# Optimization experiments

Hardware: AMD Instinct MI355X
Metric: run time of the kernel (lower is better)

The kernel has to match this reference:

```python
import jax, jax.numpy as jnp
import numpy as np

ENC, PRED, JOINT_H, VOCAB, BLANK, MAXSYM = 1024, 320, 512, 29, 28, 6


def _lstm_step(x, h, c, Wi, Wh, b):
    # torch LSTM gate order: i, f, g, o
    gates = x @ Wi.T + h @ Wh.T + b
    i, f, g, o = jnp.split(gates, 4, axis=-1)
    c2 = jax.nn.sigmoid(f) * c + jax.nn.sigmoid(i) * jnp.tanh(g)
    h2 = jax.nn.sigmoid(o) * jnp.tanh(c2)
    return h2, c2


def setup_inputs() -> dict:
    key = jax.random.key(0)
    ks = jax.random.split(key, 13)
    B, T = 32, 48
    s = 0.1
    return {
        "x": jax.random.normal(ks[0], (B, T, ENC), jnp.float32),
        "out_lens": jax.random.randint(ks[1], (B,), T // 2, T + 1),
        "emb": s * jax.random.normal(ks[2], (VOCAB - 1, PRED), jnp.float32),
        "Wi0": s * jax.random.normal(ks[3], (4 * PRED, PRED), jnp.float32),
        "Wh0": s * jax.random.normal(ks[4], (4 * PRED, PRED), jnp.float32),
        "b0": s * jax.random.normal(ks[5], (4 * PRED,), jnp.float32),
        "Wi1": s * jax.random.normal(ks[6], (4 * PRED, PRED), jnp.float32),
        "Wh1": s * jax.random.normal(ks[7], (4 * PRED, PRED), jnp.float32),
        "b1": s * jax.random.normal(ks[8], (4 * PRED,), jnp.float32),
        "Wj1": s * jax.random.normal(ks[9], (JOINT_H, ENC + PRED), jnp.float32),
        "bj1": s * jax.random.normal(ks[10], (JOINT_H,), jnp.float32),
        "Wj2": s * jax.random.normal(ks[11], (VOCAB, JOINT_H), jnp.float32),
        "bj2": s * jax.random.normal(ks[12], (VOCAB,), jnp.float32),
    }


def reference(x, out_lens, emb, Wi0, Wh0, b0, Wi1, Wh1, b1, Wj1, bj1, Wj2, bj2):
    B, T, _ = x.shape
    rows = jnp.arange(B)
    n_steps = T * MAXSYM  # upper bound on greedy-loop iterations

    def pred_step(label, h, c):
        # SOS (-1) -> zero embedding, matching model.prediction(None, ...)
        e = jnp.where((label >= 0)[:, None], emb[jnp.clip(label, 0)], 0.0)
        h0, c0 = _lstm_step(e, h[0], c[0], Wi0, Wh0, b0)
        h1, c1 = _lstm_step(h0, h[1], c[1], Wi1, Wh1, b1)
        return h1, jnp.stack([h0, h1]), jnp.stack([c0, c1])

    def joint(f, g):
        z = jnp.concatenate([f, g], axis=-1)  # [B, ENC+PRED]
        return jax.nn.relu(z @ Wj1.T + bj1) @ Wj2.T + bj2  # [B, VOCAB]

    def body(state, _):
        h, c, lt, lc, f, ti, sa = state
        last = lt[rows, lc]                      # last emitted symbol (or -1 = SOS)
        g, h_p, c_p = pred_step(last, h, c)
        logits = joint(f, g)
        k = jnp.argmax(logits, axis=-1).astype(jnp.int32)
        blankness = k == BLANK
        ti = ti + blankness.astype(jnp.int32)
        blank_vec = ti >= out_lens               # finished sequences
        sa = sa * (~blankness)                   # reset symbol count on blank
        not_blank = ~(blank_vec | blankness)
        # masked hidden-state scatter: hidden[:, idx, :] = hidden_prime[:, idx, :]
        h = jnp.where(not_blank[None, :, None], h_p, h)
        c = jnp.where(not_blank[None, :, None], c_p, c)
        lc = lc + not_blank.astype(jnp.int32)
        # index_put_ accumulate of (k - SOS) into label tensor initialized to SOS=-1
        lt = lt.at[rows, lc].add(jnp.where(not_blank, k + 1, 0))
        sa = sa + not_blank.astype(jnp.int32)
        need_add = sa >= MAXSYM                  # force time advance at max symbols
        ti = ti + need_add.astype(jnp.int32)
        sa = sa * (sa < MAXSYM)
        # data-dependent re-fetch of encoder frame (clamped like time_idxs.min(max_lens))
        f = x[rows, jnp.minimum(ti, T - 1)]
        return (h, c, lt, lc, f, ti, sa), None

    h0 = jnp.zeros((2, B, PRED), x.dtype)
    c0 = jnp.zeros((2, B, PRED), x.dtype)
    lt0 = jnp.full((B, n_steps), -1, jnp.int32)
    lc0 = jnp.zeros((B,), jnp.int32)
    ti0 = jnp.zeros((B,), jnp.int32)
    sa0 = jnp.zeros((B,), jnp.int32)
    f0 = x[:, 0, :]
    state, _ = jax.lax.scan(body, (h0, c0, lt0, lc0, f0, ti0, sa0), None, length=n_steps)
    _, _, lt, lc, _, _, _ = state
    # labels for item i are lt[i, 1:lc[i]+1]; return padded tensor + lengths
    return lt, lc
```

## Files before the change

### kernel.cpp

```cpp
#include <hip/hip_runtime.h>
#include <math.h>

#define B_ 32
#define T_ 48
#define ENC_ 1024
#define PRED_ 320
#define JH_ 512
#define NJ_ 1344
#define VOCAB_ 29
#define BLANK_ 28
#define MAXSYM_ 6
#define NSTEPS_ 288
#define BDEC 512
#define GRID_DEC 160
#define NG 8
#define GBAT 4
#define NBLK 20
#define JPB 16
#define NJB 16
#define VPB 32
#define HPAD 324

#define FPRE_OFF 0
#define WE_OFF   786432
#define H0C2_OFF 822272
#define H1C2_OFF 842752
#define PL2_OFF  863232
#define INT_OFF  928768
#define NTAGS    2560
#define STAMPF   106496

__device__ __forceinline__ float sigm(float v) { return 1.0f / (1.0f + expf(-v)); }

__device__ __forceinline__ int  ld_i(const int* p)   { return __hip_atomic_load((int*)p, __ATOMIC_RELAXED, __HIP_MEMORY_SCOPE_AGENT); }
__device__ __forceinline__ void st_i(int* p, int v)  { __hip_atomic_store(p, v, __ATOMIC_RELAXED, __HIP_MEMORY_SCOPE_AGENT); }

__device__ __forceinline__ void st_pair(float* p, float v, int stamp) {
    float2 x; x.x = v; x.y = __int_as_float(stamp);
    asm volatile("global_store_dwordx2 %0, %1, off sc0 sc1" :: "v"(p), "v"(x) : "memory");
}
__device__ __forceinline__ void ldc4_2(const float* p0, const float* p1,
                                       float4& r0, float4& r1) {
    asm volatile("global_load_dwordx4 %0, %2, off sc0 sc1\n\t"
                 "global_load_dwordx4 %1, %3, off sc0 sc1\n\t"
                 "s_waitcnt vmcnt(0)"
                 : "=&v"(r0), "=&v"(r1)
                 : "v"(p0), "v"(p1)
                 : "memory");
}
__device__ __forceinline__ void ld2x4(const float* p0, const float* p1,
                                      const float* p2, const float* p3,
                                      float2& r0, float2& r1, float2& r2, float2& r3) {
    asm volatile("global_load_dwordx2 %0, %4, off sc0 sc1\n\t"
                 "global_load_dwordx2 %1, %5, off sc0 sc1\n\t"
                 "global_load_dwordx2 %2, %6, off sc0 sc1\n\t"
                 "global_load_dwordx2 %3, %7, off sc0 sc1\n\t"
                 "s_waitcnt vmcnt(0)"
                 : "=&v"(r0), "=&v"(r1), "=&v"(r2), "=&v"(r3)
                 : "v"(p0), "v"(p1), "v"(p2), "v"(p3)
                 : "memory");
}

#define PIDX(g, ks, jl, gb) ((((g)*8 + (ks))*16 + (jl))*4 + (gb))

__global__ void k_init(float* __restrict__ ws, int* __restrict__ out) {
    int idx = blockIdx.x * blockDim.x + threadIdx.x;
    int stride = gridDim.x * blockDim.x;
    for (int i = idx; i < STAMPF; i += stride) ws[H0C2_OFF + i] = 0.0f;
    int* wi = (int*)ws;
    for (int i = idx; i < NTAGS; i += stride) wi[INT_OFF + i] = 0;
    for (int i = idx; i < B_*NSTEPS_; i += stride) out[i] = -1;
    if (idx < B_) out[B_*NSTEPS_ + idx] = 0;
}

__global__ __launch_bounds__(256) void k_we(const float* __restrict__ emb,
                                            const float* __restrict__ Wi0,
                                            float* __restrict__ ws) {
    __shared__ float es[PRED_];
    int l = blockIdx.x / 5;
    int rq = blockIdx.x % 5;
    int t = threadIdx.x;
    if (t < PRED_) es[t] = emb[l*PRED_ + t];
    if (t + 256 < PRED_) es[t + 256] = emb[l*PRED_ + t + 256];
    __syncthreads();
    int r = rq*256 + t;
    const float4* wr = (const float4*)(Wi0 + (size_t)r*PRED_);
    float acc = 0.0f;
    #pragma unroll 4
    for (int k4 = 0; k4 < PRED_/4; ++k4) {
        float4 w = wr[k4];
        acc += w.x*es[4*k4] + w.y*es[4*k4+1] + w.z*es[4*k4+2] + w.w*es[4*k4+3];
    }
    ws[WE_OFF + l*(4*PRED_) + r] = acc;
}

__global__ __launch_bounds__(256) void k_fpre(const float* __restrict__ x,
                                              const float* __restrict__ Wj1,
                                              const float* __restrict__ bj1,
                                              float* __restrict__ ws) {
    __shared__ float As[B_][129];
    __shared__ float Bs[64][129];
    int tt = blockIdx.x >> 3;
    int jb = blockIdx.x & 7;
    int tid = threadIdx.x;
    int b = tid >> 3, jq = tid & 7;
    float acc[8] = {0,0,0,0,0,0,0,0};
    for (int kc = 0; kc < ENC_; kc += 128) {
        for (int i = tid; i < B_*128; i += 256) {
            int bb = i >> 7, kk = i & 127;
            As[bb][kk] = x[((size_t)bb*T_ + tt)*ENC_ + kc + kk];
        }
        for (int i = tid; i < 64*128; i += 256) {
            int jj = i >> 7, kk = i & 127;
            Bs[jj][kk] = Wj1[((size_t)(jb*64 + jj))*NJ_ + kc + kk];
        }
        __syncthreads();
        for (int kk = 0; kk < 128; ++kk) {
            float a = As[b][kk];
            #pragma unroll
            for (int u = 0; u < 8; ++u) acc[u] += a * Bs[jq*8 + u][kk];
        }
        __syncthreads();
    }
    #pragma unroll
    for (int u = 0; u < 8; ++u) {
        int j = jb*64 + jq*8 + u;
        ws[FPRE_OFF + ((size_t)b*T_ + tt)*JH_ + j] = acc[u] + bj1[j];
    }
}

__global__ __launch_bounds__(BDEC) void k_decode(
    const int* __restrict__ out_lens,
    const float* __restrict__ Wh0, const float* __restrict__ b0,
    const float* __restrict__ Wi1, const float* __restrict__ Wh1,
    const float* __restrict__ b1,
    const float* __restrict__ Wj1,
    const float* __restrict__ Wj2, const float* __restrict__ bj2,
    float* __restrict__ ws, int* __restrict__ out)
{
    const int tid = threadIdx.x;
    const int grp = blockIdx.x & 7;
    const int lb  = blockIdx.x >> 3;
    const int j0  = lb * JPB;
    const int v0  = lb * VPB;
    const int bb0 = grp * GBAT;

    float* H0C2g = ws + H0C2_OFF + grp*2560;
    float* H1C2g = ws + H1C2_OFF + grp*2560;
    float* PL2g  = ws + PL2_OFF  + grp*8192;
    const float* WE = ws + WE_OFF;
    const float* FP = ws + FPRE_OFF;
    int* wi = (int*)ws;
    int* tagD = wi + INT_OFF + grp*320;

    __shared__ __align__(16) float wi1_s[64*HPAD];
    __shared__ __align__(16) float hs0[GBAT*HPAD];
    __shared__ __align__(16) float hs1[GBAT*HPAD];
    __shared__ float parts[2048];
    __shared__ float parts2[2048];
    __shared__ float P0a[256], P0b[256], P1s[256];
    __shared__ float c0cur[64], c0cand[64], c1cur[64], c1cand[64];
    __shared__ float we_s[28][64];
    __shared__ float b0_s[64], b1_s[64], bj2_s[32];
    __shared__ float wj2t[VPB*33];
    __shared__ float jg_c[VPB*GBAT];
    __shared__ float hid_s[GBAT*33];
    __shared__ float logits_s[GBAT*33];
    __shared__ int ti_l[GBAT], last_l[GBAT], sa_l[GBAT], lc_l[GBAT], olen_s[GBAT];
    __shared__ unsigned s_masks[2];

    for (int i = tid; i < 64*PRED_; i += BDEC) {
        int r = i / PRED_, c = i % PRED_;
        int g = r >> 4, jj = r & 15;
        wi1_s[r*HPAD + c] = Wi1[((size_t)(g*PRED_ + j0 + jj))*PRED_ + c];
    }
    if (lb < NJB) {
        for (int i = tid; i < VPB*32; i += BDEC) {
            int v = i >> 5, l = i & 31;
            wj2t[v*33 + l] = (l < VOCAB_) ? Wj2[(size_t)l*JH_ + v0 + v] : 0.f;
        }
    }
    for (int i = tid; i < 28*64; i += BDEC) {
        int ls = i >> 6, r = i & 63;
        int g = r >> 4, jj = r & 15;
        we_s[ls][r] = WE[(size_t)ls*(4*PRED_) + g*PRED_ + j0 + jj];
    }
    if (tid < 64) {
        int g = tid >> 4, jj = tid & 15;
        b0_s[tid] = b0[g*PRED_ + j0 + jj];
        b1_s[tid] = b1[g*PRED_ + j0 + jj];
        c0cur[tid]=0.f; c0cand[tid]=0.f; c1cur[tid]=0.f; c1cand[tid]=0.f;
    }
    if (tid < VOCAB_) bj2_s[tid] = bj2[tid];
    if (tid < GBAT) {
        olen_s[tid] = out_lens[bb0 + tid];
        ti_l[tid] = 0; last_l[tid] = -1; sa_l[tid] = 0; lc_l[tid] = 0;
    }
    for (int i = tid; i < GBAT*HPAD; i += BDEC) { hs0[i] = 0.f; hs1[i] = 0.f; }
    if (tid < 256) P0a[tid] = 0.f;
    __syncthreads();

    const int gb  = tid & 3;
    const int jl  = (tid >> 2) & 15;
    const int ks  = tid >> 6;
    unsigned nbm = 0xfu, actm = 0xfu;

    for (int s = 0; s < NSTEPS_; ++s) {
        const int par = s & 1;
        const int st = s + 1;

        float f_reg = 0.f;
        if (lb < NJB && tid < 128) {
            int v_ = tid & 31, g2_ = tid >> 5;
            if ((actm >> g2_) & 1) {
                int tm = min(ti_l[g2_], T_ - 1);
                f_reg = FP[((size_t)(bb0+g2_)*T_ + tm)*JH_ + v0 + v_];
            }
        }

        if (nbm) {
            if (tid < 64) {
                int g2 = tid & 3, jj = tid >> 2;
                if ((nbm >> g2) & 1) {
                    int ls = last_l[g2];
                    float gt[4];
                    #pragma unroll
                    for (int g = 0; g < 4; ++g) {
                        int r = g*16 + jj;
                        float v = P0a[r*4 + g2] + b0_s[r];
                        if (ls >= 0) v += we_s[ls][r];
                        gt[g] = v;
                    }
                    float cn = sigm(gt[1])*c0cur[tid] + sigm(gt[0])*tanhf(gt[2]);
                    float hn = sigm(gt[3])*tanhf(cn);
                    c0cand[tid] = cn;
                    hs0[g2*HPAD + j0 + jj] = hn;
                    st_pair(&H0C2g[(lb*64 + tid)*2], hn, st);
                }
            }
            {
                const float* hr = &hs1[gb*HPAD];
                int k0 = ks * 40;
                float a0=0.f,a1=0.f,a2=0.f,a3=0.f;
                const float* w0 = Wh1 + ((size_t)(0*PRED_ + j0 + jl))*PRED_;
                const float* w1 = Wh1 + ((size_t)(1*PRED_ + j0 + jl))*PRED_;
                const float* w2 = Wh1 + ((size_t)(2*PRED_ + j0 + jl))*PRED_;
                const float* w3 = Wh1 + ((size_t)(3*PRED_ + j0 + jl))*PRED_;
                #pragma unroll 10
                for (int kk = k0; kk < k0 + 40; kk += 4) {
                    float4 h = *(const float4*)&hr[kk];
                    float4 q0 = *(const float4*)(w0 + kk);
                    float4 q1 = *(const float4*)(w1 + kk);
                    float4 q2 = *(const float4*)(w2 + kk);
                    float4 q3 = *(const float4*)(w3 + kk);
                    a0 += q0.x*h.x+q0.y*h.y+q0.z*h.z+q0.w*h.w;
                    a1 += q1.x*h.x+q1.y*h.y+q1.z*h.z+q1.w*h.w;
                    a2 += q2.x*h.x+q2.y*h.y+q2.z*h.z+q2.w*h.w;
                    a3 += q3.x*h.x+q3.y*h.y+q3.z*h.z+q3.w*h.w;
                }
                parts[PIDX(0,ks,jl,gb)] = a0;
                parts[PIDX(1,ks,jl,gb)] = a1;
                parts[PIDX(2,ks,jl,gb)] = a2;
                parts[PIDX(3,ks,jl,gb)] = a3;
            }
            __syncthreads();
            if (tid < 256) {
                int r = tid >> 2, g2 = tid & 3;
                int g = r >> 4, jj = r & 15;
                float v = 0.f;
                #pragma unroll
                for (int k = 0; k < 8; ++k) v += parts[PIDX(g,k,jj,g2)];
                P1s[r*4 + g2] = v;
            }
            {
                int b = tid >> 4, jj = tid & 15;
                if (tid < 320 && b != lb) {
                    const bool n0=(nbm>>0)&1, n1=(nbm>>1)&1, n2=(nbm>>2)&1, n3=(nbm>>3)&1;
                    const float* a0 = H0C2g + tid*8;
                    const float* a1 = a0 + 4;
                    float4 r0, r1;
                    for (;;) {
                        ldc4_2(a0, a1, r0, r1);
                        bool ok = (!n0 || __float_as_int(r0.y)==st)
                               && (!n1 || __float_as_int(r0.w)==st)
                               && (!n2 || __float_as_int(r1.y)==st)
                               && (!n3 || __float_as_int(r1.w)==st);
                        if (ok) break;
                        __builtin_amdgcn_s_sleep(1);
                    }
                    if (n0) hs0[0*HPAD + b*16 + jj] = r0.x;
                    if (n1) hs0[1*HPAD + b*16 + jj] = r0.z;
                    if (n2) hs0[2*HPAD + b*16 + jj] = r1.x;
                    if (n3) hs0[3*HPAD + b*16 + jj] = r1.z;
                }
            }
            __syncthreads();

            {
                const float* hr = &hs0[gb*HPAD];
                int k0 = ks * 40;
                float a0=0.f,a1=0.f,a2=0.f,a3=0.f;
                #pragma unroll 10
                for (int kk = k0; kk < k0 + 40; kk += 4) {
                    float4 h = *(const float4*)&hr[kk];
                    float4 q0 = *(const float4*)&wi1_s[(0*16+jl)*HPAD + kk];
                    float4 q1 = *(const float4*)&wi1_s[(1*16+jl)*HPAD + kk];
                    float4 q2 = *(const float4*)&wi1_s[(2*16+jl)*HPAD + kk];
                    float4 q3 = *(const float4*)&wi1_s[(3*16+jl)*HPAD + kk];
                    a0 += q0.x*h.x+q0.y*h.y+q0.z*h.z+q0.w*h.w;
                    a1 += q1.x*h.x+q1.y*h.y+q1.z*h.z+q1.w*h.w;
                    a2 += q2.x*h.x+q2.y*h.y+q2.z*h.z+q2.w*h.w;
                    a3 += q3.x*h.x+q3.y*h.y+q3.z*h.z+q3.w*h.w;
                }
                parts[PIDX(0,ks,jl,gb)] = a0;
                parts[PIDX(1,ks,jl,gb)] = a1;
                parts[PIDX(2,ks,jl,gb)] = a2;
                parts[PIDX(3,ks,jl,gb)] = a3;
            }
            __syncthreads();
            if (tid < 64) {
                int g2 = tid & 3, jj = tid >> 2;
                if ((nbm >> g2) & 1) {
                    float gt[4];
                    #pragma unroll
                    for (int g = 0; g < 4; ++g) {
                        int r = g*16 + jj;
                        float v = P1s[r*4 + g2] + b1_s[r];
                        #pragma unroll
                        for (int k = 0; k < 8; ++k) v += parts[PIDX(g,k,jj,g2)];
                        gt[g] = v;
                    }
                    float cn = sigm(gt[1])*c1cur[tid] + sigm(gt[0])*tanhf(gt[2]);
                    float hn = sigm(gt[3])*tanhf(cn);
                    c1cand[tid] = cn;
                    hs1[g2*HPAD + j0 + jj] = hn;
                    st_pair(&H1C2g[(lb*64 + tid)*2], hn, st);
                }
            }
            {
                const float* hr = &hs0[gb*HPAD];
                int k0 = ks * 40;
                float a0=0.f,a1=0.f,a2=0.f,a3=0.f;
                const float* w0 = Wh0 + ((size_t)(0*PRED_ + j0 + jl))*PRED_;
                const float* w1 = Wh0 + ((size_t)(1*PRED_ + j0 + jl))*PRED_;
                const float* w2 = Wh0 + ((size_t)(2*PRED_ + j0 + jl))*PRED_;
                const float* w3 = Wh0 + ((size_t)(3*PRED_ + j0 + jl))*PRED_;
                #pragma unroll 10
                for (int kk = k0; kk < k0 + 40; kk += 4) {
                    float4 h = *(const float4*)&hr[kk];
                    float4 q0 = *(const float4*)(w0 + kk);
                    float4 q1 = *(const float4*)(w1 + kk);
                    float4 q2 = *(const float4*)(w2 + kk);
                    float4 q3 = *(const float4*)(w3 + kk);
                    a0 += q0.x*h.x+q0.y*h.y+q0.z*h.z+q0.w*h.w;
                    a1 += q1.x*h.x+q1.y*h.y+q1.z*h.z+q1.w*h.w;
                    a2 += q2.x*h.x+q2.y*h.y+q2.z*h.z+q2.w*h.w;
                    a3 += q3.x*h.x+q3.y*h.y+q3.z*h.z+q3.w*h.w;
                }
                parts2[PIDX(0,ks,jl,gb)] = a0;
                parts2[PIDX(1,ks,jl,gb)] = a1;
                parts2[PIDX(2,ks,jl,gb)] = a2;
                parts2[PIDX(3,ks,jl,gb)] = a3;
            }
            {
                int b = tid >> 4, jj = tid & 15;
                if (tid < 320 && b != lb) {
                    const bool n0=(nbm>>0)&1, n1=(nbm>>1)&1, n2=(nbm>>2)&1, n3=(nbm>>3)&1;
                    const float* a0 = H1C2g + tid*8;
                    const float* a1 = a0 + 4;
                    float4 r0, r1;
                    for (;;) {
                        ldc4_2(a0, a1, r0, r1);
                        bool ok = (!n0 || __float_as_int(r0.y)==st)
                               && (!n1 || __float_as_int(r0.w)==st)
                               && (!n2 || __float_as_int(r1.y)==st)
                               && (!n3 || __float_as_int(r1.w)==st);
                        if (ok) break;
                        __builtin_amdgcn_s_sleep(1);
                    }
                    if (n0) hs1[0*HPAD + b*16 + jj] = r0.x;
                    if (n1) hs1[1*HPAD + b*16 + jj] = r0.z;
                    if (n2) hs1[2*HPAD + b*16 + jj] = r1.x;
                    if (n3) hs1[3*HPAD + b*16 + jj] = r1.z;
                }
            }
            __syncthreads();
        } else {
            if (lb < NJB) {
                if (tid < NBLK) { while (ld_i(&tagD[tid*16]) < s-1) __builtin_amdgcn_s_sleep(1); }
                __syncthreads();
            }
        }

        if (lb < NJB) {
            if (nbm) {
                int v = tid & 31, g2 = (tid >> 5) & 3, ks2 = tid >> 7;
                if ((nbm >> g2) & 1) {
                    const float* hr = &hs1[g2*HPAD];
                    const float* wt = Wj1 + ((size_t)(v0 + v))*NJ_ + ENC_ + ks2*80;
                    const float* hk = hr + ks2*80;
                    float p = 0.f;
                    #pragma unroll 20
                    for (int kk = 0; kk < 80; kk += 4) {
                        float4 w4 = *(const float4*)(wt + kk);
                        float4 h  = *(const float4*)(hk + kk);
                        p += w4.x*h.x + w4.y*h.y + w4.z*h.z + w4.w*h.w;
                    }
                    parts[(v*4 + g2)*4 + ks2] = p;
                }
            }
            __syncthreads();
            if (tid < 128) {
                int v = tid & 31, g2 = tid >> 5;
                if (nbm && ((nbm >> g2) & 1)) {
                    jg_c[v*4 + g2] = parts[(v*4+g2)*4+0] + parts[(v*4+g2)*4+1]
                                   + parts[(v*4+g2)*4+2] + parts[(v*4+g2)*4+3];
                }
                if ((actm >> g2) & 1) {
                    hid_s[g2*33 + v] = fmaxf(f_reg + jg_c[v*4 + g2], 0.f);
                }
            }
            __syncthreads();
            if (tid < 128) {
                int g2 = tid >> 5, l = tid & 31;
                const float* hb = &hid_s[g2*33];
                float acc = 0.f;
                #pragma unroll 8
                for (int v = 0; v < VPB; ++v) acc += wj2t[v*33 + l] * hb[v];
                st_pair(&PL2g[par*4096 + (lb*128 + tid)*2], acc, st);
            }
        }

        if (nbm && tid < 256) {
            int r = tid >> 2, g2 = tid & 3;
            int g = r >> 4, jj = r & 15;
            float v = 0.f;
            #pragma unroll
            for (int k = 0; k < 8; ++k) v += parts2[PIDX(g,k,jj,g2)];
            P0b[r*4 + g2] = v;
        }

        {
            int lb4 = tid >> 7, slot = tid & 127;
            const float* base = PL2g + par*4096 + (lb4*4*128 + slot)*2;
            float2 q0, q1, q2, q3;
            for (;;) {
                ld2x4(base, base + 256, base + 512, base + 768, q0, q1, q2, q3);
                if (__float_as_int(q0.y)==st && __float_as_int(q1.y)==st &&
                    __float_as_int(q2.y)==st && __float_as_int(q3.y)==st) break;
                __builtin_amdgcn_s_sleep(1);
            }
            parts[tid] = ((q0.x + q1.x) + q2.x) + q3.x;
        }
        __syncthreads();
        if (tid < 128) {
            float v = ((parts[tid] + parts[128+tid]) + parts[256+tid]) + parts[384+tid];
            int g2 = tid >> 5, l = tid & 31;
            logits_s[g2*33 + l] = (l < VOCAB_) ? (v + bj2_s[l]) : -1e30f;
        }
        __syncthreads();

        if (tid < 64) {
            bool nbb = false, actb = false;
            if (tid < GBAT && ((actm >> tid) & 1)) {
                const int g2 = tid;
                float best = -1e30f; int bi = 0;
                for (int l = 0; l < VOCAB_; ++l) {
                    float v = logits_s[g2*33 + l];
                    if (v > best) { best = v; bi = l; }
                }
                const int blankness = (bi == BLANK_) ? 1 : 0;
                int tiv = ti_l[g2] + blankness;
                if (tiv >= olen_s[g2]) {
                    ti_l[g2] = tiv;
                } else {
                    int notb = 1 - blankness;
                    int sav = blankness ? 0 : sa_l[g2];
                    int nl = last_l[g2];
                    int lcn = lc_l[g2];
                    if (notb) {
                        lcn += 1;
                        if (lb == g2) {
                            int bglob = bb0 + g2;
                            if (lcn < NSTEPS_) st_i(&out[bglob*NSTEPS_ + lcn], bi);
                            st_i(&out[B_*NSTEPS_ + bglob], lcn);
                        }
                        nl = bi;
                        sav += 1;
                    }
                    if (sav >= MAXSYM_) { tiv += 1; sav = 0; }
                    ti_l[g2] = tiv; sa_l[g2] = sav; last_l[g2] = nl; lc_l[g2] = lcn;
                    nbb = (notb != 0); actb = true;
                }
            }
            unsigned long long bn = __ballot(nbb);
            unsigned long long ba = __ballot(actb);
            if (tid == 0) { s_masks[0] = (unsigned)bn; s_masks[1] = (unsigned)ba; }
        }
        __syncthreads();
        const unsigned nbm_new = s_masks[0];
        actm = s_masks[1];
        if (tid < 64) {
            if ((nbm_new >> (tid & 3)) & 1) { c0cur[tid] = c0cand[tid]; c1cur[tid] = c1cand[tid]; }
        }
        if (tid < 256) {
            if ((nbm_new >> (tid & 3)) & 1) P0a[tid] = P0b[tid];
        }
        __syncthreads();
        nbm = nbm_new;
        if (tid == 0) st_i(&tagD[lb*16], s + 1);
        if (!actm) break;
    }
}

extern "C" void kernel_launch(void* const* d_in, const int* in_sizes, int n_in,
                              void* d_out, int out_size, void* d_ws, size_t ws_size,
                              hipStream_t stream) {
    const float* x    = (const float*)d_in[0];
    const int*   olen = (const int*)d_in[1];
    const float* emb  = (const float*)d_in[2];
    const float* Wi0  = (const float*)d_in[3];
    const float* Wh0  = (const float*)d_in[4];
    const float* b0   = (const float*)d_in[5];
    const float* Wi1  = (const float*)d_in[6];
    const float* Wh1  = (const float*)d_in[7];
    const float* b1   = (const float*)d_in[8];
    const float* Wj1  = (const float*)d_in[9];
    const float* bj1  = (const float*)d_in[10];
    const float* Wj2  = (const float*)d_in[11];
    const float* bj2  = (const float*)d_in[12];
    float* ws = (float*)d_ws;
    int* out = (int*)d_out;

    hipLaunchKernelGGL(k_init, dim3(256), dim3(256), 0, stream, ws, out);
    hipLaunchKernelGGL(k_we,   dim3(28*5), dim3(256), 0, stream, emb, Wi0, ws);
    hipLaunchKernelGGL(k_fpre, dim3(T_*8), dim3(256), 0, stream, x, Wj1, bj1, ws);
    hipLaunchKernelGGL(k_decode, dim3(GRID_DEC), dim3(BDEC), 0, stream,
                       olen, Wh0, b0, Wi1, Wh1, b1, Wj1, Wj2, bj2, ws, out);
}
```

Baseline: 4.422 ms.

## Restructure cross-block polling and overlap Wh1 matvec with logits gather

Cross-block spin-wait loads for the layer-0 and layer-1 hidden states are consolidated onto 128 threads, each polling five contiguous dwordx4 slots. The reductions of partial sums run concurrently on the other threads. The Wh1 recurrent matvec for the next step moves after the joint stage so it overlaps the logits exchange. The logits gather now reads contiguous vectors and reduces over 16 partials, with parts zeroed at init. The intent is fewer barriers and less serialized polling latency per greedy step. The cost is reordered data dependencies and an extra barrier before the layer-1 gather.

New measurement: 5.819 ms. 1.32x slower.

```diff
diff --git a/kernel.cpp b/kernel.cpp
--- a/kernel.cpp
+++ b/kernel.cpp
@@ -39,25 +39,29 @@
     float2 x; x.x = v; x.y = __int_as_float(stamp);
     asm volatile("global_store_dwordx2 %0, %1, off sc0 sc1" :: "v"(p), "v"(x) : "memory");
 }
-__device__ __forceinline__ void ldc4_2(const float* p0, const float* p1,
-                                       float4& r0, float4& r1) {
-    asm volatile("global_load_dwordx4 %0, %2, off sc0 sc1\n\t"
-                 "global_load_dwordx4 %1, %3, off sc0 sc1\n\t"
-                 "s_waitcnt vmcnt(0)"
-                 : "=&v"(r0), "=&v"(r1)
-                 : "v"(p0), "v"(p1)
-                 : "memory");
-}
-__device__ __forceinline__ void ld2x4(const float* p0, const float* p1,
-                                      const float* p2, const float* p3,
-                                      float2& r0, float2& r1, float2& r2, float2& r3) {
-    asm volatile("global_load_dwordx2 %0, %4, off sc0 sc1\n\t"
-                 "global_load_dwordx2 %1, %5, off sc0 sc1\n\t"
-                 "global_load_dwordx2 %2, %6, off sc0 sc1\n\t"
-                 "global_load_dwordx2 %3, %7, off sc0 sc1\n\t"
+__device__ __forceinline__ void ldc4_4(const float* p0, const float* p1,
+                                       const float* p2, const float* p3,
+                                       float4& r0, float4& r1, float4& r2, float4& r3) {
+    asm volatile("global_load_dwordx4 %0, %4, off sc0 sc1\n\t"
+                 "global_load_dwordx4 %1, %5, off sc0 sc1\n\t"
+                 "global_load_dwordx4 %2, %6, off sc0 sc1\n\t"
+                 "global_load_dwordx4 %3, %7, off sc0 sc1\n\t"
                  "s_waitcnt vmcnt(0)"
                  : "=&v"(r0), "=&v"(r1), "=&v"(r2), "=&v"(r3)
                  : "v"(p0), "v"(p1), "v"(p2), "v"(p3)
+                 : "memory");
+}
+__device__ __forceinline__ void ldc4_5(const float* p0, const float* p1, const float* p2,
+                                       const float* p3, const float* p4,
+                                       float4& r0, float4& r1, float4& r2, float4& r3, float4& r4) {
+    asm volatile("global_load_dwordx4 %0, %5, off sc0 sc1\n\t"
+                 "global_load_dwordx4 %1, %6, off sc0 sc1\n\t"
+                 "global_load_dwordx4 %2, %7, off sc0 sc1\n\t"
+                 "global_load_dwordx4 %3, %8, off sc0 sc1\n\t"
+                 "global_load_dwordx4 %4, %9, off sc0 sc1\n\t"
+                 "s_waitcnt vmcnt(0)"
+                 : "=&v"(r0), "=&v"(r1), "=&v"(r2), "=&v"(r3), "=&v"(r4)
+                 : "v"(p0), "v"(p1), "v"(p2), "v"(p3), "v"(p4)
                  : "memory");
 }
 
@@ -198,6 +202,7 @@
     }
     for (int i = tid; i < GBAT*HPAD; i += BDEC) { hs0[i] = 0.f; hs1[i] = 0.f; }
     if (tid < 256) P0a[tid] = 0.f;
+    for (int i = tid; i < 2048; i += BDEC) parts[i] = 0.f;
     __syncthreads();
 
     const int gb  = tid & 3;
@@ -238,61 +243,40 @@
                     st_pair(&H0C2g[(lb*64 + tid)*2], hn, st);
                 }
             }
-            {
-                const float* hr = &hs1[gb*HPAD];
-                int k0 = ks * 40;
-                float a0=0.f,a1=0.f,a2=0.f,a3=0.f;
-                const float* w0 = Wh1 + ((size_t)(0*PRED_ + j0 + jl))*PRED_;
-                const float* w1 = Wh1 + ((size_t)(1*PRED_ + j0 + jl))*PRED_;
-                const float* w2 = Wh1 + ((size_t)(2*PRED_ + j0 + jl))*PRED_;
-                const float* w3 = Wh1 + ((size_t)(3*PRED_ + j0 + jl))*PRED_;
-                #pragma unroll 10
-                for (int kk = k0; kk < k0 + 40; kk += 4) {
-                    float4 h = *(const float4*)&hr[kk];
-                    float4 q0 = *(const float4*)(w0 + kk);
-                    float4 q1 = *(const float4*)(w1 + kk);
-                    float4 q2 = *(const float4*)(w2 + kk);
-                    float4 q3 = *(const float4*)(w3 + kk);
-                    a0 += q0.x*h.x+q0.y*h.y+q0.z*h.z+q0.w*h.w;
-                    a1 += q1.x*h.x+q1.y*h.y+q1.z*h.z+q1.w*h.w;
-                    a2 += q2.x*h.x+q2.y*h.y+q2.z*h.z+q2.w*h.w;
-                    a3 += q3.x*h.x+q3.y*h.y+q3.z*h.z+q3.w*h.w;
-                }
-                parts[PIDX(0,ks,jl,gb)] = a0;
-                parts[PIDX(1,ks,jl,gb)] = a1;
-                parts[PIDX(2,ks,jl,gb)] = a2;
-                parts[PIDX(3,ks,jl,gb)] = a3;
-            }
-            __syncthreads();
-            if (tid < 256) {
-                int r = tid >> 2, g2 = tid & 3;
+            if (tid < 128) {
+                int p0 = tid * 10;
+                const float* base = H0C2g + p0*2;
+                bool nd[10];
+                #pragma unroll
+                for (int i = 0; i < 10; ++i) {
+                    int p = p0 + i;
+                    nd[i] = (((nbm >> (p & 3)) & 1) != 0) && ((p >> 6) != lb);
+                }
+                float4 r0, r1, r2, r3, r4;
+                for (;;) {
+                    ldc4_5(base, base+4, base+8, base+12, base+16, r0, r1, r2, r3, r4);
+                    bool ok = (!nd[0] || __float_as_int(r0.y)==st) && (!nd[1] || __float_as_int(r0.w)==st)
+                           && (!nd[2] || __float_as_int(r1.y)==st) && (!nd[3] || __float_as_int(r1.w)==st)
+                           && (!nd[4] || __float_as_int(r2.y)==st) && (!nd[5] || __float_as_int(r2.w)==st)
+                           && (!nd[6] || __float_as_int(r3.y)==st) && (!nd[7] || __float_as_int(r3.w)==st)
+                           && (!nd[8] || __float_as_int(r4.y)==st) && (!nd[9] || __float_as_int(r4.w)==st);
+                    if (ok) break;
+                    __builtin_amdgcn_s_sleep(1);
+                }
+                float vv[10] = {r0.x,r0.z,r1.x,r1.z,r2.x,r2.z,r3.x,r3.z,r4.x,r4.z};
+                #pragma unroll
+                for (int i = 0; i < 10; ++i) {
+                    int p = p0 + i;
+                    if (nd[i]) hs0[(p&3)*HPAD + (p>>6)*16 + ((p&63)>>2)] = vv[i];
+                }
+            } else if (tid < 384) {
+                int t = tid - 128;
+                int r = t >> 2, g2 = t & 3;
                 int g = r >> 4, jj = r & 15;
                 float v = 0.f;
                 #pragma unroll
                 for (int k = 0; k < 8; ++k) v += parts[PIDX(g,k,jj,g2)];
                 P1s[r*4 + g2] = v;
-            }
-            {
-                int b = tid >> 4, jj = tid & 15;
-                if (tid < 320 && b != lb) {
-                    const bool n0=(nbm>>0)&1, n1=(nbm>>1)&1, n2=(nbm>>2)&1, n3=(nbm>>3)&1;
-                    const float* a0 = H0C2g + tid*8;
-                    const float* a1 = a0 + 4;
-                    float4 r0, r1;
-                    for (;;) {
-                        ldc4_2(a0, a1, r0, r1);
-                        bool ok = (!n0 || __float_as_int(r0.y)==st)
-                               && (!n1 || __float_as_int(r0.w)==st)
-                               && (!n2 || __float_as_int(r1.y)==st)
-                               && (!n3 || __float_as_int(r1.w)==st);
-                        if (ok) break;
-                        __builtin_amdgcn_s_sleep(1);
-                    }
-                    if (n0) hs0[0*HPAD + b*16 + jj] = r0.x;
-                    if (n1) hs0[1*HPAD + b*16 + jj] = r0.z;
-                    if (n2) hs0[2*HPAD + b*16 + jj] = r1.x;
-                    if (n3) hs0[3*HPAD + b*16 + jj] = r1.z;
-                }
             }
             __syncthreads();
 
@@ -362,27 +346,41 @@
                 parts2[PIDX(2,ks,jl,gb)] = a2;
                 parts2[PIDX(3,ks,jl,gb)] = a3;
             }
-            {
-                int b = tid >> 4, jj = tid & 15;
-                if (tid < 320 && b != lb) {
-                    const bool n0=(nbm>>0)&1, n1=(nbm>>1)&1, n2=(nbm>>2)&1, n3=(nbm>>3)&1;
-                    const float* a0 = H1C2g + tid*8;
-                    const float* a1 = a0 + 4;
-                    float4 r0, r1;
-                    for (;;) {
-                        ldc4_2(a0, a1, r0, r1);
-                        bool ok = (!n0 || __float_as_int(r0.y)==st)
-                               && (!n1 || __float_as_int(r0.w)==st)
-                               && (!n2 || __float_as_int(r1.y)==st)
-                               && (!n3 || __float_as_int(r1.w)==st);
-                        if (ok) break;
-                        __builtin_amdgcn_s_sleep(1);
-                    }
-                    if (n0) hs1[0*HPAD + b*16 + jj] = r0.x;
-                    if (n1) hs1[1*HPAD + b*16 + jj] = r0.z;
-                    if (n2) hs1[2*HPAD + b*16 + jj] = r1.x;
-                    if (n3) hs1[3*HPAD + b*16 + jj] = r1.z;
-                }
+            __syncthreads();
+            if (tid < 128) {
+                int p0 = tid * 10;
+                const float* base = H1C2g + p0*2;
+                bool nd[10];
+                #pragma unroll
+                for (int i = 0; i < 10; ++i) {
+                    int p = p0 + i;
+                    nd[i] = (((nbm >> (p & 3)) & 1) != 0) && ((p >> 6) != lb);
+                }
+                float4 r0, r1, r2, r3, r4;
+                for (;;) {
+                    ldc4_5(base, base+4, base+8, base+12, base+16, r0, r1, r2, r3, r4);
+                    bool ok = (!nd[0] || __float_as_int(r0.y)==st) && (!nd[1] || __float_as_int(r0.w)==st)
+                           && (!nd[2] || __float_as_int(r1.y)==st) && (!nd[3] || __float_as_int(r1.w)==st)
+                           && (!nd[4] || __float_as_int(r2.y)==st) && (!nd[5] || __float_as_int(r2.w)==st)
+                           && (!nd[6] || __float_as_int(r3.y)==st) && (!nd[7] || __float_as_int(r3.w)==st)
+                           && (!nd[8] || __float_as_int(r4.y)==st) && (!nd[9] || __float_as_int(r4.w)==st);
+                    if (ok) break;
+                    __builtin_amdgcn_s_sleep(1);
+                }
+                float vv[10] = {r0.x,r0.z,r1.x,r1.z,r2.x,r2.z,r3.x,r3.z,r4.x,r4.z};
+                #pragma unroll
+                for (int i = 0; i < 10; ++i) {
+                    int p = p0 + i;
+                    if (nd[i]) hs1[(p&3)*HPAD + (p>>6)*16 + ((p&63)>>2)] = vv[i];
+                }
+            } else if (tid >= 256) {
+                int t = tid - 256;
+                int r = t >> 2, g2 = t & 3;
+                int g = r >> 4, jj = r & 15;
+                float v = 0.f;
+                #pragma unroll
+                for (int k = 0; k < 8; ++k) v += parts2[PIDX(g,k,jj,g2)];
+                P0b[r*4 + g2] = v;
             }
             __syncthreads();
         } else {
@@ -431,30 +429,52 @@
             }
         }
 
-        if (nbm && tid < 256) {
-            int r = tid >> 2, g2 = tid & 3;
-            int g = r >> 4, jj = r & 15;
+        {
+            const float* hr = &hs1[gb*HPAD];
+            int k0 = ks * 40;
+            float a0=0.f,a1=0.f,a2=0.f,a3=0.f;
+            const float* w0 = Wh1 + ((size_t)(0*PRED_ + j0 + jl))*PRED_;
+            const float* w1 = Wh1 + ((size_t)(1*PRED_ + j0 + jl))*PRED_;
+            const float* w2 = Wh1 + ((size_t)(2*PRED_ + j0 + jl))*PRED_;
+            const float* w3 = Wh1 + ((size_t)(3*PRED_ + j0 + jl))*PRED_;
+            #pragma unroll 10
+            for (int kk = k0; kk < k0 + 40; kk += 4) {
+                float4 h = *(const float4*)&hr[kk];
+                float4 q0 = *(const float4*)(w0 + kk);
+                float4 q1 = *(const float4*)(w1 + kk);
+                float4 q2 = *(const float4*)(w2 + kk);
+                float4 q3 = *(const float4*)(w3 + kk);
+                a0 += q0.x*h.x+q0.y*h.y+q0.z*h.z+q0.w*h.w;
+                a1 += q1.x*h.x+q1.y*h.y+q1.z*h.z+q1.w*h.w;
+                a2 += q2.x*h.x+q2.y*h.y+q2.z*h.z+q2.w*h.w;
+                a3 += q3.x*h.x+q3.y*h.y+q3.z*h.z+q3.w*h.w;
+            }
+            parts[PIDX(0,ks,jl,gb)] = a0;
+            parts[PIDX(1,ks,jl,gb)] = a1;
+            parts[PIDX(2,ks,jl,gb)] = a2;
+            parts[PIDX(3,ks,jl,gb)] = a3;
+        }
+
+        if (tid < 256) {
+            int p0 = tid * 8;
+            const float* base = PL2g + par*4096 + p0*2;
+            float4 q0, q1, q2, q3;
+            for (;;) {
+                ldc4_4(base, base+4, base+8, base+12, q0, q1, q2, q3);
+                if (__float_as_int(q0.y)==st && __float_as_int(q0.w)==st &&
+                    __float_as_int(q1.y)==st && __float_as_int(q1.w)==st &&
+                    __float_as_int(q2.y)==st && __float_as_int(q2.w)==st &&
+                    __float_as_int(q3.y)==st && __float_as_int(q3.w)==st) break;
+                __builtin_amdgcn_s_sleep(1);
+            }
+            parts2[p0+0]=q0.x; parts2[p0+1]=q0.z; parts2[p0+2]=q1.x; parts2[p0+3]=q1.z;
+            parts2[p0+4]=q2.x; parts2[p0+5]=q2.z; parts2[p0+6]=q3.x; parts2[p0+7]=q3.z;
+        }
+        __syncthreads();
+        if (tid < 128) {
             float v = 0.f;
             #pragma unroll
-            for (int k = 0; k < 8; ++k) v += parts2[PIDX(g,k,jj,g2)];
-            P0b[r*4 + g2] = v;
-        }
-
-        {
-            int lb4 = tid >> 7, slot = tid & 127;
-            const float* base = PL2g + par*4096 + (lb4*4*128 + slot)*2;
-            float2 q0, q1, q2, q3;
-            for (;;) {
-                ld2x4(base, base + 256, base + 512, base + 768, q0, q1, q2, q3);
-                if (__float_as_int(q0.y)==st && __float_as_int(q1.y)==st &&
-                    __float_as_int(q2.y)==st && __float_as_int(q3.y)==st) break;
-                __builtin_amdgcn_s_sleep(1);
-            }
-            parts[tid] = ((q0.x + q1.x) + q2.x) + q3.x;
-        }
-        __syncthreads();
-        if (tid < 128) {
-            float v = ((parts[tid] + parts[128+tid]) + parts[256+tid]) + parts[384+tid];
+            for (int k = 0; k < 16; ++k) v += parts2[k*128 + tid];
             int g2 = tid >> 5, l = tid & 31;
             logits_s[g2*33 + l] = (l < VOCAB_) ? (v + bj2_s[l]) : -1e30f;
         }
```
